# Optimization experiments

Measured on AMD Instinct MI355X. Metric: run time of the kernel, lower is better.

The kernel has to match this reference:

```python
import jax, jax.numpy as jnp
import numpy as np

B, N, E = 64, 1024, 16384   # graphs, nodes/graph, edges/graph
F, H, T, C = 128, 64, 10, 2 # input_dim, hid_dim, token_num, num_classes
INNER_PRUNE, CROSS_PRUNE = 0.3, 0.1
NEG_SLOPE = 0.01            # ProG act() defaults to leaky_relu


def setup_inputs() -> dict:
    key = jax.random.key(0)
    ks = jax.random.split(key, 8)
    x = jax.random.normal(ks[0], (B, N, F), jnp.float32)
    edge_src = jax.random.randint(ks[1], (B, E), 0, N, jnp.int32)
    edge_dst = jax.random.randint(ks[2], (B, E), 0, N, jnp.int32)
    # kaiming_uniform(leaky_relu, a=0.01, fan_in) for prompt tokens
    bound = float(np.sqrt(6.0 / ((1.0 + NEG_SLOPE ** 2) * F)))
    tokens = jax.random.uniform(ks[3], (T, F), jnp.float32, -bound, bound)

    def lin(k, fi, fo):
        b = 1.0 / np.sqrt(fi)
        k1, k2 = jax.random.split(k)
        return (jax.random.uniform(k1, (fi, fo), jnp.float32, -b, b),
                jax.random.uniform(k2, (fo,), jnp.float32, -b, b))

    W1, b1 = lin(ks[4], F, H)   # GCNConv 1
    W2, b2 = lin(ks[5], H, H)   # GCNConv 2
    Wa, ba = lin(ks[6], H, C)   # answering head
    return dict(x=x, tokens=tokens, W1=W1, b1=b1, W2=W2, b2=b2,
                Wa=Wa, ba=ba, edge_src=edge_src, edge_dst=edge_dst)


def reference(x, tokens, W1, b1, W2, b2, Wa, ba, edge_src, edge_dst):
    dt = x.dtype
    # --- HeavyPrompt: thresholded adjacency (edge existence only; PyG GCNConv
    # is called without edge_weight, so the sim values / edge_attr are unused)
    M_in = (jax.nn.sigmoid(tokens @ tokens.T) >= INNER_PRUNE).astype(dt)          # [T,T]
    M_cr = (jax.nn.sigmoid(jnp.einsum('tf,bnf->btn', tokens, x)) >= CROSS_PRUNE).astype(dt)  # [B,T,N], token->node

    # --- GCN normalization with self-loops (deg over targets)
    deg_tok = 1.0 + M_in.sum(0)                                                   # [T] (tokens only receive inner edges)
    offs = (jnp.arange(B, dtype=edge_dst.dtype) * N)[:, None]
    src_g = (edge_src + offs).reshape(-1)                                         # [B*E] global node ids
    dst_g = (edge_dst + offs).reshape(-1)
    in_deg = jax.ops.segment_sum(jnp.ones_like(dst_g, dt), dst_g, B * N).reshape(B, N)
    deg_node = 1.0 + in_deg + M_cr.sum(1)                                         # [B,N]
    inv_s_tok = jax.lax.rsqrt(deg_tok)
    inv_s_node = jax.lax.rsqrt(deg_node)
    inv_node_flat = inv_s_node.reshape(-1)
    norm_in = M_in * inv_s_tok[:, None] * inv_s_tok[None, :]                      # [T,T]
    ew = inv_node_flat[src_g] * inv_node_flat[dst_g]                              # per-edge 1/sqrt(di*dj)

    def gcn(ht, hn, W, b):
        # GCNConv: linear -> normalized aggregation (incl. self loop) -> +bias
        ht = ht @ W                                                               # [T,Fo] (token stream is graph-independent)
        hn = jnp.einsum('bnf,fo->bno', hn, W)                                     # [B,N,Fo]
        out_tok = norm_in @ ht + ht * (1.0 / deg_tok)[:, None] + b
        hn_flat = hn.reshape(B * N, -1)
        agg = jax.ops.segment_sum(hn_flat[src_g] * ew[:, None], dst_g, B * N).reshape(B, N, -1)
        cross = jnp.einsum('btn,to->bno', M_cr * inv_s_tok[None, :, None], ht) * inv_s_node[..., None]
        out_node = agg + cross + hn * (1.0 / deg_node)[..., None] + b
        return out_tok, out_node

    ht, hn = gcn(tokens, x, W1, b1)
    lrelu = lambda v: jnp.where(v >= 0, v, NEG_SLOPE * v)                         # act(); dropout is eval no-op
    ht, hn = lrelu(ht), lrelu(hn)
    ht, hn = gcn(ht, hn, W2, b2)                                                  # node_emb
    # global_mean_pool over each prompted graph (T tokens + N nodes)
    graph_emb = (ht.sum(0)[None, :] + hn.sum(1)) / (T + N)                        # [B,H]
    return jax.nn.softmax(graph_emb @ Wa + ba, axis=1)                            # answering
```

## Files before the change

kernel.cpp:

```cpp
#include <hip/hip_runtime.h>
#include <hip/hip_bf16.h>
#include <stdint.h>

#define B_ 64
#define N_ 1024
#define E_ 16384
#define F_ 128
#define H_ 64
#define T_ 10
#define BN (B_*N_)
#define BE (B_*E_)

#define TH_INNER (-0.84729786f)
#define TH_CROSS (-2.1972246f)

typedef __attribute__((ext_vector_type(8))) short short8;
typedef __attribute__((ext_vector_type(4))) float f32x4;

__device__ __forceinline__ float ld1(const void* p, int i, int bf) {
    if (bf) {
        uint16_t u = ((const uint16_t*)p)[i];
        return __uint_as_float(((uint32_t)u) << 16);
    }
    return ((const float*)p)[i];
}

__device__ __forceinline__ short to_bf(float x) {
    return (short)__bfloat16_as_ushort(__float2bfloat16(x));
}

__device__ __forceinline__ uint32_t pack_bf2(float lo, float hi) {
    uint32_t l = (uint32_t)__bfloat16_as_ushort(__float2bfloat16(lo));
    uint32_t h = (uint32_t)__bfloat16_as_ushort(__float2bfloat16(hi));
    return l | (h << 16);
}

__device__ __forceinline__ float bflo(uint32_t u) { return __uint_as_float(u << 16); }
__device__ __forceinline__ float bfhi(uint32_t u) { return __uint_as_float(u & 0xffff0000u); }

__global__ __launch_bounds__(1024) void k_count_prep(const int* __restrict__ dst,
                                                     int* __restrict__ cnt4,
                                                     const void* __restrict__ W1,
                                                     const void* __restrict__ W2,
                                                     const void* __restrict__ tokens,
                                                     int* __restrict__ flag,
                                                     short8* __restrict__ Bfr,
                                                     short8* __restrict__ Bfr2,
                                                     float* __restrict__ gsum,
                                                     uint32_t* __restrict__ y1pad,
                                                     uint32_t* __restrict__ y2pad) {
    __shared__ int lcnt[N_];
    int t = threadIdx.x;
    if (blockIdx.x >= 256) {
        uint32_t du = ((const uint32_t*)tokens)[t & 63];
        float dlo = __uint_as_float(du << 16);
        unsigned long long vote = __ballot(fabsf(dlo) <= 1.0f);
        int bf = (vote == ~0ull) ? 1 : 0;
        if (blockIdx.x == 256 && t == 0) *flag = bf;
        int f = (int)(blockIdx.x - 256) * 1024 + t;
        if (f < 1280) {
            int c = f / 320, rem = f % 320;
            int nt = rem / 64, lane = rem % 64;
            int q = lane >> 4, n = nt * 16 + (lane & 15);
            int k0 = c * 32 + q * 8;
            short8 v;
#pragma unroll
            for (int j = 0; j < 8; ++j) {
                int k = k0 + j;
                float x = 0.f;
                if (n < H_) x = ld1(W1, k * H_ + n, bf);
                else if (n < H_ + T_) x = ld1(tokens, (n - H_) * F_ + k, bf);
                v[j] = to_bf(x);
            }
            Bfr[f] = v;
        } else if (f < 1792) {
            int f2 = f - 1280;
            int c = f2 / 256, rem = f2 % 256;
            int nt = rem / 64, lane = rem % 64;
            int q = lane >> 4, n = nt * 16 + (lane & 15);
            int k0 = c * 32 + q * 8;
            short8 v;
#pragma unroll
            for (int j = 0; j < 8; ++j) v[j] = to_bf(ld1(W2, (k0 + j) * H_ + n, bf));
            Bfr2[f2] = v;
        }
        return;
    }
    int g = blockIdx.x & 63, c = blockIdx.x >> 6;
    lcnt[t] = 0;
    if (c == 0 && t < 64) gsum[g * 64 + t] = 0.f;
    if (blockIdx.x == 0) {
        if (t < 32) y1pad[t] = 0;
        else if (t < 64) y2pad[t - 32] = 0;
    }
    __syncthreads();
#pragma unroll
    for (int it = 0; it < 4; ++it)
        atomicAdd(&lcnt[dst[g * E_ + c * 4096 + it * 1024 + t]], 1);
    __syncthreads();
    cnt4[c * BN + g * N_ + t] = lcnt[t];
}

__global__ __launch_bounds__(1024) void k_scan_tok(const int* __restrict__ cnt4,
                                                   int* __restrict__ cnt,
                                                   int* __restrict__ offs,
                                                   int* __restrict__ base4,
                                                   const void* __restrict__ tokens,
                                                   const void* __restrict__ b1,
                                                   const void* __restrict__ b2,
                                                   const short8* __restrict__ Bfr,
                                                   const short8* __restrict__ Bfr2,
                                                   const int* __restrict__ flag,
                                                   uint32_t* __restrict__ y1,
                                                   uint32_t* __restrict__ y2,
                                                   float* __restrict__ tok_sum) {
    __shared__ int wsum[16];
    __shared__ float nm[T_ * 16];
    __shared__ float ist_s[16], idt_s[16];
    __shared__ float htbuf[T_ * 64];
    __shared__ float h1s[T_ * 64];
    int t = threadIdx.x;
    if (blockIdx.x < 64) {
        int g = blockIdx.x;
        int c0 = cnt4[0 * BN + g * N_ + t];
        int c1 = cnt4[1 * BN + g * N_ + t];
        int c2 = cnt4[2 * BN + g * N_ + t];
        int c3 = cnt4[3 * BN + g * N_ + t];
        int v = c0 + c1 + c2 + c3;
        int sc = v;
#pragma unroll
        for (int d = 1; d < 64; d <<= 1) {
            int u = __shfl_up(sc, d);
            if ((t & 63) >= d) sc += u;
        }
        if ((t & 63) == 63) wsum[t >> 6] = sc;
        __syncthreads();
        if (t < 16) {
            int wsc = wsum[t];
#pragma unroll
            for (int d = 1; d < 16; d <<= 1) {
                int u = __shfl_up(wsc, d);
                if (t >= d) wsc += u;
            }
            wsum[t] = wsc;
        }
        __syncthreads();
        int base = sc - v + ((t >= 64) ? wsum[(t >> 6) - 1] : 0);
        int o = g * E_ + base;
        cnt[g * N_ + t] = v;
        offs[g * N_ + t] = o;
        base4[0 * BN + g * N_ + t] = o;
        base4[1 * BN + g * N_ + t] = o + c0;
        base4[2 * BN + g * N_ + t] = o + c0 + c1;
        base4[3 * BN + g * N_ + t] = o + c0 + c1 + c2;
        return;
    }
    int bf = *flag;
    int l = t;
    bool act = (l < 64);
    int m = l & 15, q = (l & 63) >> 4;
    int mrow = (m < T_) ? m : (T_ - 1);
    f32x4 accM = {};
    f32x4 acc1[4] = {};
    float istc = 0.f, idtc = 0.f;
    if (act) {
        short8 afr[4];
        if (bf) {
            const short8* ar = (const short8*)((const uint16_t*)tokens + mrow * F_);
#pragma unroll
            for (int c = 0; c < 4; ++c) afr[c] = ar[c * 4 + q];
        } else {
            const float* ar = (const float*)tokens + mrow * F_;
#pragma unroll
            for (int c = 0; c < 4; ++c)
#pragma unroll
                for (int j = 0; j < 8; ++j) afr[c][j] = to_bf(ar[c * 32 + q * 8 + j]);
        }
#pragma unroll
        for (int c = 0; c < 4; ++c) {
            accM = __builtin_amdgcn_mfma_f32_16x16x32_bf16(afr[c], Bfr[(c * 5 + 4) * 64 + l], accM, 0, 0, 0);
#pragma unroll
            for (int nt = 0; nt < 4; ++nt)
                acc1[nt] = __builtin_amdgcn_mfma_f32_16x16x32_bf16(afr[c], Bfr[(c * 5 + nt) * 64 + l], acc1[nt], 0, 0, 0);
        }
        int ccnt = 0;
#pragma unroll
        for (int r = 0; r < 4; ++r) {
            int row = q * 4 + r;
            if (row < T_ && m < T_ && accM[r] >= TH_INNER) ccnt++;
        }
        ccnt += __shfl_xor(ccnt, 16);
        ccnt += __shfl_xor(ccnt, 32);
        float deg = 1.f + (float)ccnt;
        istc = 1.f / sqrtf(deg);
        idtc = 1.f / deg;
        if (q == 0 && m < T_) { ist_s[m] = istc; idt_s[m] = idtc; }
#pragma unroll
        for (int nt = 0; nt < 4; ++nt)
#pragma unroll
            for (int r = 0; r < 4; ++r) {
                int row = q * 4 + r;
                if (row < T_) htbuf[row * 64 + nt * 16 + m] = acc1[nt][r];
            }
    }
    __syncthreads();
    if (act && m < T_) {
#pragma unroll
        for (int r = 0; r < 4; ++r) {
            int row = q * 4 + r;
            if (row < T_)
                nm[row * 16 + m] = (accM[r] >= TH_INNER) ? ist_s[row] * istc : 0.f;
        }
    }
    __syncthreads();
    if (act) {
        float htc[T_];
#pragma unroll
        for (int s = 0; s < T_; ++s) htc[s] = htbuf[s * 64 + l];
        float b1f = ld1(b1, l, bf);
#pragma unroll
        for (int tt = 0; tt < T_; ++tt) {
            float a = htc[tt] * idt_s[tt] + b1f;
#pragma unroll
            for (int s = 0; s < T_; ++s) a += nm[tt * 16 + s] * htc[s];
            a = (a >= 0.f) ? a : 0.01f * a;
            h1s[tt * 64 + l] = a;
            float v = ist_s[tt] * htc[tt];
            float vh = __shfl(v, l + 1);
            if ((l & 1) == 0) y1[(size_t)(BN + 1 + tt) * 32 + (l >> 1)] = pack_bf2(v, vh);
        }
    }
    __syncthreads();
    if (act) {
        short8 a2fr[2];
#pragma unroll
        for (int c = 0; c < 2; ++c)
#pragma unroll
            for (int j = 0; j < 8; ++j) a2fr[c][j] = to_bf(h1s[mrow * 64 + c * 32 + q * 8 + j]);
        f32x4 acc2[4] = {};
#pragma unroll
        for (int nt = 0; nt < 4; ++nt)
#pragma unroll
            for (int c = 0; c < 2; ++c)
                acc2[nt] = __builtin_amdgcn_mfma_f32_16x16x32_bf16(a2fr[c], Bfr2[(c * 4 + nt) * 64 + l], acc2[nt], 0, 0, 0);
#pragma unroll
        for (int nt = 0; nt < 4; ++nt)
#pragma unroll
            for (int r = 0; r < 4; ++r) {
                int row = q * 4 + r;
                if (row < T_) htbuf[row * 64 + nt * 16 + m] = acc2[nt][r];
            }
    }
    __syncthreads();
    if (act) {
        float htc[T_];
#pragma unroll
        for (int s = 0; s < T_; ++s) htc[s] = htbuf[s * 64 + l];
        float b2f = ld1(b2, l, bf);
        float ts = 0.f;
#pragma unroll
        for (int tt = 0; tt < T_; ++tt) {
            float o = htc[tt] * idt_s[tt] + b2f;
#pragma unroll
            for (int s = 0; s < T_; ++s) o += nm[tt * 16 + s] * htc[s];
            ts += o;
            float v = ist_s[tt] * htc[tt];
            float vh = __shfl(v, l + 1);
            if ((l & 1) == 0) y2[(size_t)(BN + 1 + tt) * 32 + (l >> 1)] = pack_bf2(v, vh);
        }
        tok_sum[l] = ts;
    }
}

__global__ __launch_bounds__(1024) void k_scatter(const int* __restrict__ src,
                                                  const int* __restrict__ dst,
                                                  const int* __restrict__ base4,
                                                  int* __restrict__ bucket) {
    __shared__ int cur[N_];
    int t = threadIdx.x;
    int g = blockIdx.x & 63, c = blockIdx.x >> 6;
    cur[t] = base4[c * BN + g * N_ + t];
    __syncthreads();
#pragma unroll
    for (int it = 0; it < 4; ++it) {
        int i = g * E_ + c * 4096 + it * 1024 + t;
        int d = dst[i];
        int p = atomicAdd(&cur[d], 1);
        bucket[p] = g * N_ + src[i];
    }
}

__global__ __launch_bounds__(256) void k_node_mfma(const void* __restrict__ x,
                                                   const short8* __restrict__ Bfr,
                                                   const int* __restrict__ cnt,
                                                   const int* __restrict__ flag,
                                                   uint32_t* __restrict__ y1,
                                                   float* __restrict__ inv_s,
                                                   int* __restrict__ maskA) {
    int bf = *flag;
    int tid = threadIdx.x;
    int lane = tid & 63, wv = tid >> 6;
    int g = blockIdx.x & 63, c = blockIdx.x >> 6;
    int row0 = g * N_ + c * 64 + wv * 16;
    int m = lane & 15, q = lane >> 4;
    int row = row0 + m;
    short8 afr[4];
    if (bf) {
        const short8* ar = (const short8*)((const uint16_t*)x + (size_t)row * F_);
#pragma unroll
        for (int cc = 0; cc < 4; ++cc) afr[cc] = ar[cc * 4 + q];
    } else {
        const float* ar = (const float*)x + (size_t)row * F_;
#pragma unroll
        for (int cc = 0; cc < 4; ++cc)
#pragma unroll
            for (int j = 0; j < 8; ++j)
                afr[cc][j] = to_bf(ar[cc * 32 + q * 8 + j]);
    }
    f32x4 acc[5] = {};
#pragma unroll
    for (int nt = 0; nt < 5; ++nt)
#pragma unroll
        for (int cc = 0; cc < 4; ++cc) {
            short8 bfr = Bfr[(cc * 5 + nt) * 64 + lane];
            acc[nt] = __builtin_amdgcn_mfma_f32_16x16x32_bf16(afr[cc], bfr, acc[nt], 0, 0, 0);
        }
    unsigned long long bal[4];
#pragma unroll
    for (int r = 0; r < 4; ++r) {
        int pred = (m < T_) && (acc[4][r] >= TH_CROSS);
        bal[r] = __ballot(pred);
    }
    float isv[4];
#pragma unroll
    for (int r = 0; r < 4; ++r) {
        int node = row0 + q * 4 + r;
        int mk = (int)((bal[r] >> (q * 16)) & 0x3FF);
        int ec = cnt[node];
        int pc = __popc((unsigned)mk);
        float deg = 1.f + (float)ec + (float)pc;
        isv[r] = 1.f / sqrtf(deg);
        if (m == 0) { inv_s[node] = isv[r]; maskA[node] = mk; }
    }
#pragma unroll
    for (int r = 0; r < 4; ++r) {
        int node = row0 + q * 4 + r;
#pragma unroll
        for (int nt = 0; nt < 4; ++nt) {
            float v = acc[nt][r] * isv[r];
            float vh = __shfl(v, lane + 1);
            if ((m & 1) == 0)
                y1[(size_t)node * 32 + nt * 8 + (m >> 1)] = pack_bf2(v, vh);
        }
    }
}

#define NROWS (N_ + 12)

__device__ __forceinline__ void stage_slice(uint32_t* __restrict__ ys,
                                            const uint32_t* __restrict__ yg,
                                            const uint32_t* __restrict__ yall,
                                            int tid) {
#pragma unroll
    for (int it = 0; it < 9; ++it) {
        int idx = it * 1024 + tid;
        if (idx < NROWS * 8) {
            int r = idx >> 3, gg = idx & 7;
            const uint32_t* sp = (r < N_) ? (yg + r * 32)
                                          : (yall + (size_t)(BN + (r - N_)) * 32);
            *(uint4*)&ys[r * 32 + gg * 4] = *(const uint4*)(sp + gg * 4);
        }
    }
}

__device__ __forceinline__ void gather_grp(const uint32_t* __restrict__ ys,
                                           const int* __restrict__ bucket,
                                           int cnt_g, int off_g, int msk_g, int self_l,
                                           int wp, float a[8]) {
#pragma unroll
    for (int j = 0; j < 8; ++j) a[j] = 0.f;
    int cm = cnt_g;
    cm = max(cm, __shfl_xor(cm, 8));
    cm = max(cm, __shfl_xor(cm, 16));
    cm = max(cm, __shfl_xor(cm, 32));
    int nid0 = (cnt_g > 0) ? bucket[off_g] : 0;
    int nid1 = (cnt_g > 1) ? bucket[off_g + 1] : 0;
    for (int e = 0; e < cm; ++e) {
        int cur = nid0;
        nid0 = nid1;
        if (e + 2 < cnt_g) nid1 = bucket[off_g + e + 2];
        if (e < cnt_g) {
            int sl = cur & (N_ - 1);
            uint4 u = *(const uint4*)&ys[sl * 32 + wp * 4];
            a[0] += bflo(u.x); a[1] += bfhi(u.x);
            a[2] += bflo(u.y); a[3] += bfhi(u.y);
            a[4] += bflo(u.z); a[5] += bfhi(u.z);
            a[6] += bflo(u.w); a[7] += bfhi(u.w);
        }
    }
    unsigned mm = (unsigned)msk_g;
    while (mm) {
        int tk = __ffs(mm) - 1;
        mm &= mm - 1;
        uint4 u = *(const uint4*)&ys[(N_ + 1 + tk) * 32 + wp * 4];
        a[0] += bflo(u.x); a[1] += bfhi(u.x);
        a[2] += bflo(u.y); a[3] += bfhi(u.y);
        a[4] += bflo(u.z); a[5] += bfhi(u.z);
        a[6] += bflo(u.w); a[7] += bfhi(u.w);
    }
    {
        uint4 u = *(const uint4*)&ys[self_l * 32 + wp * 4];
        a[0] += bflo(u.x); a[1] += bfhi(u.x);
        a[2] += bflo(u.y); a[3] += bfhi(u.y);
        a[4] += bflo(u.z); a[5] += bfhi(u.z);
        a[6] += bflo(u.w); a[7] += bfhi(u.w);
    }
}

__global__ __launch_bounds__(1024, 1) void k_layer1(const uint32_t* __restrict__ y1,
                                                    const float* __restrict__ inv_s,
                                                    const int* __restrict__ cnt,
                                                    const int* __restrict__ offs,
                                                    const int* __restrict__ maskA,
                                                    const int* __restrict__ bucket,
                                                    const void* __restrict__ b1,
                                                    const short8* __restrict__ Bfr2,
                                                    const int* __restrict__ flag,
                                                    uint32_t* __restrict__ y2) {
    __shared__ uint32_t y1s[NROWS * 32];
    __shared__ uint32_t h1w[16][9 * 36];
    int bf = *flag;
    int tid = threadIdx.x;
    int lane = tid & 63, wv = tid >> 6;
    int gi = lane >> 3, wp = lane & 7;
    int g = blockIdx.x & 63, c = blockIdx.x >> 6;
    stage_slice(y1s, y1 + (size_t)g * N_ * 32, y1, tid);
    int nbase = g * N_ + c * 256 + wv * 16;
    int ln16 = lane & 15;
    int cntv = cnt[nbase + ln16];
    int offv = offs[nbase + ln16];
    float isvv = inv_s[nbase + ln16];
    int mskv = maskA[nbase + ln16];
    float bc[8];
#pragma unroll
    for (int j = 0; j < 8; ++j) bc[j] = ld1(b1, wp * 8 + j, bf);
    if (lane < 36) h1w[wv][8 * 36 + lane] = 0;
    __syncthreads();
    int m = lane & 15, q = lane >> 4;
    int mr = (m < 8) ? m : 8;
    for (int k = 0; k < 2; ++k) {
        int ni = k * 8 + gi;
        int cnt_g = __shfl(cntv, ni);
        int off_g = __shfl(offv, ni);
        int msk_g = __shfl(mskv, ni);
        float is_g = __shfl(isvv, ni);
        float a[8];
        gather_grp(y1s, bucket, cnt_g, off_g, msk_g, c * 256 + wv * 16 + ni, wp, a);
        uint32_t pk[4];
#pragma unroll
        for (int j = 0; j < 4; ++j) {
            float h0 = a[2 * j] * is_g + bc[2 * j];
            float h1v = a[2 * j + 1] * is_g + bc[2 * j + 1];
            h0 = (h0 >= 0.f) ? h0 : 0.01f * h0;
            h1v = (h1v >= 0.f) ? h1v : 0.01f * h1v;
            pk[j] = pack_bf2(h0, h1v);
        }
#pragma unroll
        for (int j = 0; j < 4; ++j) h1w[wv][gi * 36 + wp * 4 + j] = pk[j];
        short8 afr[2];
#pragma unroll
        for (int cc = 0; cc < 2; ++cc)
            afr[cc] = *(const short8*)&h1w[wv][mr * 36 + cc * 16 + q * 4];
        f32x4 acc[4] = {};
#pragma unroll
        for (int nt = 0; nt < 4; ++nt)
#pragma unroll
            for (int cc = 0; cc < 2; ++cc)
                acc[nt] = __builtin_amdgcn_mfma_f32_16x16x32_bf16(afr[cc], Bfr2[(cc * 4 + nt) * 64 + lane], acc[nt], 0, 0, 0);
#pragma unroll
        for (int r = 0; r < 4; ++r) {
            int tr = q * 4 + r;
            if (tr < 8) {
                int node = nbase + k * 8 + tr;
                float is = __shfl(isvv, k * 8 + tr);
#pragma unroll
                for (int nt = 0; nt < 4; ++nt) {
                    float v = acc[nt][r] * is;
                    float vh = __shfl(v, lane + 1);
                    if ((m & 1) == 0)
                        y2[(size_t)node * 32 + nt * 8 + (m >> 1)] = pack_bf2(v, vh);
                }
            }
        }
    }
}

__global__ __launch_bounds__(1024, 1) void k_layer2(const uint32_t* __restrict__ y2,
                                                    const float* __restrict__ inv_s,
                                                    const int* __restrict__ cnt,
                                                    const int* __restrict__ offs,
                                                    const int* __restrict__ maskA,
                                                    const int* __restrict__ bucket,
                                                    const void* __restrict__ b2,
                                                    const int* __restrict__ flag,
                                                    float* __restrict__ graph_sum) {
    __shared__ uint32_t y2s[NROWS * 32];
    __shared__ float pool[16][64];
    int bf = *flag;
    int tid = threadIdx.x;
    int lane = tid & 63, wv = tid >> 6;
    int gi = lane >> 3, wp = lane & 7;
    int g = blockIdx.x & 63, c = blockIdx.x >> 6;
    stage_slice(y2s, y2 + (size_t)g * N_ * 32, y2, tid);
    int nbase = g * N_ + c * 256 + wv * 16;
    int ln16 = lane & 15;
    int cntv = cnt[nbase + ln16];
    int offv = offs[nbase + ln16];
    float isvv = inv_s[nbase + ln16];
    int mskv = maskA[nbase + ln16];
    float bc[8];
#pragma unroll
    for (int j = 0; j < 8; ++j) bc[j] = ld1(b2, wp * 8 + j, bf);
    __syncthreads();
    float p[8];
#pragma unroll
    for (int j = 0; j < 8; ++j) p[j] = 0.f;
    for (int k = 0; k < 2; ++k) {
        int ni = k * 8 + gi;
        int cnt_g = __shfl(cntv, ni);
        int off_g = __shfl(offv, ni);
        int msk_g = __shfl(mskv, ni);
        float is_g = __shfl(isvv, ni);
        float a[8];
        gather_grp(y2s, bucket, cnt_g, off_g, msk_g, c * 256 + wv * 16 + ni, wp, a);
#pragma unroll
        for (int j = 0; j < 8; ++j) p[j] += a[j] * is_g + bc[j];
    }
#pragma unroll
    for (int j = 0; j < 8; ++j) {
        p[j] += __shfl_xor(p[j], 8);
        p[j] += __shfl_xor(p[j], 16);
        p[j] += __shfl_xor(p[j], 32);
    }
    if (gi == 0) {
#pragma unroll
        for (int j = 0; j < 8; ++j) pool[wv][wp * 8 + j] = p[j];
    }
    __syncthreads();
    if (tid < 64) {
        float s = 0.f;
#pragma unroll
        for (int w2 = 0; w2 < 16; ++w2) s += pool[w2][tid];
        atomicAdd(&graph_sum[g * H_ + tid], s);
    }
}

__global__ __launch_bounds__(64) void k_final(const float* __restrict__ graph_sum,
                                              const float* __restrict__ tok_sum,
                                              const void* __restrict__ Wa,
                                              const void* __restrict__ ba,
                                              const int* __restrict__ flag,
                                              void* __restrict__ out) {
    int bf = *flag;
    int b = blockIdx.x, l = threadIdx.x;
    float e = (tok_sum[l] + graph_sum[b * H_ + l]) * (1.0f / 1034.0f);
    float p0 = e * ld1(Wa, l * 2 + 0, bf);
    float p1 = e * ld1(Wa, l * 2 + 1, bf);
#pragma unroll
    for (int d = 32; d >= 1; d >>= 1) {
        p0 += __shfl_xor(p0, d);
        p1 += __shfl_xor(p1, d);
    }
    if (l == 0) {
        float l0 = p0 + ld1(ba, 0, bf);
        float l1 = p1 + ld1(ba, 1, bf);
        float mx = fmaxf(l0, l1);
        float e0 = expf(l0 - mx), e1 = expf(l1 - mx);
        float s = e0 + e1;
        float o0 = e0 / s, o1 = e1 / s;
        if (bf) {
            ((__hip_bfloat16*)out)[b * 2 + 0] = __float2bfloat16(o0);
            ((__hip_bfloat16*)out)[b * 2 + 1] = __float2bfloat16(o1);
        } else {
            ((float*)out)[b * 2 + 0] = o0;
            ((float*)out)[b * 2 + 1] = o1;
        }
    }
}

extern "C" void kernel_launch(void* const* d_in, const int* in_sizes, int n_in,
                              void* d_out, int out_size, void* d_ws, size_t ws_size,
                              hipStream_t stream) {
    (void)in_sizes; (void)n_in; (void)out_size; (void)ws_size;
    const void* x      = d_in[0];
    const void* tokens = d_in[1];
    const void* W1     = d_in[2];
    const void* b1     = d_in[3];
    const void* W2     = d_in[4];
    const void* b2     = d_in[5];
    const void* Wa     = d_in[6];
    const void* ba     = d_in[7];
    const int* esrc = (const int*)d_in[8];
    const int* edst = (const int*)d_in[9];

    char* w = (char*)d_ws;
    auto alloc = [&](size_t bytes) { void* p = (void*)w; w += (bytes + 255) & ~(size_t)255; return p; };
    int*      cnt       = (int*)alloc(BN * 4);
    int*      offs      = (int*)alloc(BN * 4);
    int*      maskA     = (int*)alloc(BN * 4);
    float*    inv_s     = (float*)alloc(BN * 4);
    int*      cnt4      = (int*)alloc((size_t)4 * BN * 4);
    int*      base4     = (int*)alloc((size_t)4 * BN * 4);
    int*      bucket    = (int*)alloc((size_t)BE * 4 + 512);
    uint32_t* y1        = (uint32_t*)alloc((size_t)(BN + 12) * 32 * 4);
    uint32_t* y2        = (uint32_t*)alloc((size_t)(BN + 12) * 32 * 4);
    float*    tok_sum   = (float*)alloc(H_ * 4);
    float*    graph_sum = (float*)alloc(B_ * H_ * 4);
    short8*   Bfr       = (short8*)alloc(4 * 5 * 64 * sizeof(short8));
    short8*   Bfr2      = (short8*)alloc(2 * 4 * 64 * sizeof(short8));
    int*      dflag     = (int*)alloc(256);

    k_count_prep<<<258, 1024, 0, stream>>>(edst, cnt4, W1, W2, tokens, dflag, Bfr, Bfr2,
                                           graph_sum, y1 + (size_t)BN * 32, y2 + (size_t)BN * 32);
    k_scan_tok  <<<65, 1024, 0, stream>>>(cnt4, cnt, offs, base4, tokens, b1, b2,
                                          Bfr, Bfr2, dflag, y1, y2, tok_sum);
    k_scatter   <<<256, 1024, 0, stream>>>(esrc, edst, base4, bucket);
    k_node_mfma <<<BN / 64, 256, 0, stream>>>(x, Bfr, cnt, dflag, y1, inv_s, maskA);
    k_layer1    <<<B_ * 4, 1024, 0, stream>>>(y1, inv_s, cnt, offs, maskA, bucket, b1, Bfr2, dflag, y2);
    k_layer2    <<<B_ * 4, 1024, 0, stream>>>(y2, inv_s, cnt, offs, maskA, bucket, b2, dflag, graph_sum);
    k_final     <<<B_, 64, 0, stream>>>(graph_sum, tok_sum, Wa, ba, dflag, d_out);
}
```

Baseline: 160.0 us.

## Fuse scatter with node MFMA and fold final softmax into layer2 via tickets

Merges the edge-scatter kernel and the node MFMA projection into one launch with block-index dispatch, moving the MFMA part to 1024-thread blocks covering 256 rows each. The final softmax head now runs inside layer2: the last of four blocks per graph, found with a ticket counter, computes the output. The neighbour-gather loop also drops its wave-wide max-count loop bound and per-iteration guard. Together these remove two kernel launches and some divergent iterations, at the cost of an atomic ticket, a threadfence and larger node blocks with possibly lower occupancy.

```diff
diff --git a/kernel.cpp b/kernel.cpp
--- a/kernel.cpp
+++ b/kernel.cpp
@@ -47,6 +47,7 @@
                                                      short8* __restrict__ Bfr,
                                                      short8* __restrict__ Bfr2,
                                                      float* __restrict__ gsum,
+                                                     int* __restrict__ done,
                                                      uint32_t* __restrict__ y1pad,
                                                      uint32_t* __restrict__ y2pad) {
     __shared__ int lcnt[N_];
@@ -92,6 +93,7 @@
     if (blockIdx.x == 0) {
         if (t < 32) y1pad[t] = 0;
         else if (t < 64) y2pad[t - 32] = 0;
+        else if (t >= 128 && t < 192) done[t - 128] = 0;
     }
     __syncthreads();
 #pragma unroll
@@ -162,7 +164,7 @@
     int mrow = (m < T_) ? m : (T_ - 1);
     f32x4 accM = {};
     f32x4 acc1[4] = {};
-    float istc = 0.f, idtc = 0.f;
+    float istc = 0.f;
     if (act) {
         short8 afr[4];
         if (bf) {
@@ -193,8 +195,7 @@
         ccnt += __shfl_xor(ccnt, 32);
         float deg = 1.f + (float)ccnt;
         istc = 1.f / sqrtf(deg);
-        idtc = 1.f / deg;
-        if (q == 0 && m < T_) { ist_s[m] = istc; idt_s[m] = idtc; }
+        if (q == 0 && m < T_) { ist_s[m] = istc; idt_s[m] = 1.f / deg; }
 #pragma unroll
         for (int nt = 0; nt < 4; ++nt)
 #pragma unroll
@@ -272,36 +273,37 @@
     }
 }
 
-__global__ __launch_bounds__(1024) void k_scatter(const int* __restrict__ src,
-                                                  const int* __restrict__ dst,
-                                                  const int* __restrict__ base4,
-                                                  int* __restrict__ bucket) {
+__global__ __launch_bounds__(1024) void k_scatter_node(const int* __restrict__ src,
+                                                       const int* __restrict__ dst,
+                                                       const int* __restrict__ base4,
+                                                       int* __restrict__ bucket,
+                                                       const void* __restrict__ x,
+                                                       const short8* __restrict__ Bfr,
+                                                       const int* __restrict__ cnt,
+                                                       const int* __restrict__ flag,
+                                                       uint32_t* __restrict__ y1,
+                                                       float* __restrict__ inv_s,
+                                                       int* __restrict__ maskA) {
     __shared__ int cur[N_];
     int t = threadIdx.x;
-    int g = blockIdx.x & 63, c = blockIdx.x >> 6;
-    cur[t] = base4[c * BN + g * N_ + t];
-    __syncthreads();
-#pragma unroll
-    for (int it = 0; it < 4; ++it) {
-        int i = g * E_ + c * 4096 + it * 1024 + t;
-        int d = dst[i];
-        int p = atomicAdd(&cur[d], 1);
-        bucket[p] = g * N_ + src[i];
-    }
-}
-
-__global__ __launch_bounds__(256) void k_node_mfma(const void* __restrict__ x,
-                                                   const short8* __restrict__ Bfr,
-                                                   const int* __restrict__ cnt,
-                                                   const int* __restrict__ flag,
-                                                   uint32_t* __restrict__ y1,
-                                                   float* __restrict__ inv_s,
-                                                   int* __restrict__ maskA) {
+    if (blockIdx.x < 256) {
+        int g = blockIdx.x & 63, c = blockIdx.x >> 6;
+        cur[t] = base4[c * BN + g * N_ + t];
+        __syncthreads();
+#pragma unroll
+        for (int it = 0; it < 4; ++it) {
+            int i = g * E_ + c * 4096 + it * 1024 + t;
+            int d = dst[i];
+            int p = atomicAdd(&cur[d], 1);
+            bucket[p] = g * N_ + src[i];
+        }
+        return;
+    }
+    int bid = blockIdx.x - 256;
     int bf = *flag;
-    int tid = threadIdx.x;
-    int lane = tid & 63, wv = tid >> 6;
-    int g = blockIdx.x & 63, c = blockIdx.x >> 6;
-    int row0 = g * N_ + c * 64 + wv * 16;
+    int lane = t & 63, w16 = t >> 6;
+    int g = bid & 63, c = bid >> 6;
+    int row0 = g * N_ + c * 256 + w16 * 16;
     int m = lane & 15, q = lane >> 4;
     int row = row0 + m;
     short8 afr[4];
@@ -379,24 +381,18 @@
                                            int wp, float a[8]) {
 #pragma unroll
     for (int j = 0; j < 8; ++j) a[j] = 0.f;
-    int cm = cnt_g;
-    cm = max(cm, __shfl_xor(cm, 8));
-    cm = max(cm, __shfl_xor(cm, 16));
-    cm = max(cm, __shfl_xor(cm, 32));
     int nid0 = (cnt_g > 0) ? bucket[off_g] : 0;
     int nid1 = (cnt_g > 1) ? bucket[off_g + 1] : 0;
-    for (int e = 0; e < cm; ++e) {
-        int cur = nid0;
+    for (int e = 0; e < cnt_g; ++e) {
+        int curN = nid0;
         nid0 = nid1;
         if (e + 2 < cnt_g) nid1 = bucket[off_g + e + 2];
-        if (e < cnt_g) {
-            int sl = cur & (N_ - 1);
-            uint4 u = *(const uint4*)&ys[sl * 32 + wp * 4];
-            a[0] += bflo(u.x); a[1] += bfhi(u.x);
-            a[2] += bflo(u.y); a[3] += bfhi(u.y);
-            a[4] += bflo(u.z); a[5] += bfhi(u.z);
-            a[6] += bflo(u.w); a[7] += bfhi(u.w);
-        }
+        int sl = curN & (N_ - 1);
+        uint4 u = *(const uint4*)&ys[sl * 32 + wp * 4];
+        a[0] += bflo(u.x); a[1] += bfhi(u.x);
+        a[2] += bflo(u.y); a[3] += bfhi(u.y);
+        a[4] += bflo(u.z); a[5] += bfhi(u.z);
+        a[6] += bflo(u.w); a[7] += bfhi(u.w);
     }
     unsigned mm = (unsigned)msk_g;
     while (mm) {
@@ -503,9 +499,15 @@
                                                     const int* __restrict__ bucket,
                                                     const void* __restrict__ b2,
                                                     const int* __restrict__ flag,
-                                                    float* __restrict__ graph_sum) {
+                                                    float* __restrict__ graph_sum,
+                                                    int* __restrict__ done,
+                                                    const float* __restrict__ tok_sum,
+                                                    const void* __restrict__ Wa,
+                                                    const void* __restrict__ ba,
+                                                    void* __restrict__ out) {
     __shared__ uint32_t y2s[NROWS * 32];
     __shared__ float pool[16][64];
+    __shared__ int ticket_s;
     int bf = *flag;
     int tid = threadIdx.x;
     int lane = tid & 63, wv = tid >> 6;
@@ -553,37 +555,34 @@
         for (int w2 = 0; w2 < 16; ++w2) s += pool[w2][tid];
         atomicAdd(&graph_sum[g * H_ + tid], s);
     }
-}
-
-__global__ __launch_bounds__(64) void k_final(const float* __restrict__ graph_sum,
-                                              const float* __restrict__ tok_sum,
-                                              const void* __restrict__ Wa,
-                                              const void* __restrict__ ba,
-                                              const int* __restrict__ flag,
-                                              void* __restrict__ out) {
-    int bf = *flag;
-    int b = blockIdx.x, l = threadIdx.x;
-    float e = (tok_sum[l] + graph_sum[b * H_ + l]) * (1.0f / 1034.0f);
-    float p0 = e * ld1(Wa, l * 2 + 0, bf);
-    float p1 = e * ld1(Wa, l * 2 + 1, bf);
-#pragma unroll
-    for (int d = 32; d >= 1; d >>= 1) {
-        p0 += __shfl_xor(p0, d);
-        p1 += __shfl_xor(p1, d);
-    }
-    if (l == 0) {
-        float l0 = p0 + ld1(ba, 0, bf);
-        float l1 = p1 + ld1(ba, 1, bf);
-        float mx = fmaxf(l0, l1);
-        float e0 = expf(l0 - mx), e1 = expf(l1 - mx);
-        float s = e0 + e1;
-        float o0 = e0 / s, o1 = e1 / s;
-        if (bf) {
-            ((__hip_bfloat16*)out)[b * 2 + 0] = __float2bfloat16(o0);
-            ((__hip_bfloat16*)out)[b * 2 + 1] = __float2bfloat16(o1);
-        } else {
-            ((float*)out)[b * 2 + 0] = o0;
-            ((float*)out)[b * 2 + 1] = o1;
+    __threadfence();
+    if (tid == 0) ticket_s = atomicAdd(&done[g], 1);
+    __syncthreads();
+    if (ticket_s == 3 && tid < 64) {
+        int l = tid;
+        float gs = atomicAdd(&graph_sum[g * H_ + l], 0.0f);
+        float e = (tok_sum[l] + gs) * (1.0f / 1034.0f);
+        float p0 = e * ld1(Wa, l * 2 + 0, bf);
+        float p1 = e * ld1(Wa, l * 2 + 1, bf);
+#pragma unroll
+        for (int d = 32; d >= 1; d >>= 1) {
+            p0 += __shfl_xor(p0, d);
+            p1 += __shfl_xor(p1, d);
+        }
+        if (l == 0) {
+            float l0 = p0 + ld1(ba, 0, bf);
+            float l1 = p1 + ld1(ba, 1, bf);
+            float mx = fmaxf(l0, l1);
+            float e0 = expf(l0 - mx), e1 = expf(l1 - mx);
+            float s = e0 + e1;
+            float o0 = e0 / s, o1 = e1 / s;
+            if (bf) {
+                ((__hip_bfloat16*)out)[g * 2 + 0] = __float2bfloat16(o0);
+                ((__hip_bfloat16*)out)[g * 2 + 1] = __float2bfloat16(o1);
+            } else {
+                ((float*)out)[g * 2 + 0] = o0;
+                ((float*)out)[g * 2 + 1] = o1;
+            }
         }
     }
 }
@@ -616,17 +615,19 @@
     uint32_t* y2        = (uint32_t*)alloc((size_t)(BN + 12) * 32 * 4);
     float*    tok_sum   = (float*)alloc(H_ * 4);
     float*    graph_sum = (float*)alloc(B_ * H_ * 4);
+    int*      done      = (int*)alloc(B_ * 4);
     short8*   Bfr       = (short8*)alloc(4 * 5 * 64 * sizeof(short8));
     short8*   Bfr2      = (short8*)alloc(2 * 4 * 64 * sizeof(short8));
     int*      dflag     = (int*)alloc(256);
 
-    k_count_prep<<<258, 1024, 0, stream>>>(edst, cnt4, W1, W2, tokens, dflag, Bfr, Bfr2,
-                                           graph_sum, y1 + (size_t)BN * 32, y2 + (size_t)BN * 32);
-    k_scan_tok  <<<65, 1024, 0, stream>>>(cnt4, cnt, offs, base4, tokens, b1, b2,
-                                          Bfr, Bfr2, dflag, y1, y2, tok_sum);
-    k_scatter   <<<256, 1024, 0, stream>>>(esrc, edst, base4, bucket);
-    k_node_mfma <<<BN / 64, 256, 0, stream>>>(x, Bfr, cnt, dflag, y1, inv_s, maskA);
-    k_layer1    <<<B_ * 4, 1024, 0, stream>>>(y1, inv_s, cnt, offs, maskA, bucket, b1, Bfr2, dflag, y2);
-    k_layer2    <<<B_ * 4, 1024, 0, stream>>>(y2, inv_s, cnt, offs, maskA, bucket, b2, dflag, graph_sum);
-    k_final     <<<B_, 64, 0, stream>>>(graph_sum, tok_sum, Wa, ba, dflag, d_out);
-}
+    k_count_prep  <<<258, 1024, 0, stream>>>(edst, cnt4, W1, W2, tokens, dflag, Bfr, Bfr2,
+                                             graph_sum, done,
+                                             y1 + (size_t)BN * 32, y2 + (size_t)BN * 32);
+    k_scan_tok    <<<65, 1024, 0, stream>>>(cnt4, cnt, offs, base4, tokens, b1, b2,
+                                            Bfr, Bfr2, dflag, y1, y2, tok_sum);
+    k_scatter_node<<<512, 1024, 0, stream>>>(esrc, edst, base4, bucket, x, Bfr, cnt,
+                                             dflag, y1, inv_s, maskA);
+    k_layer1      <<<B_ * 4, 1024, 0, stream>>>(y1, inv_s, cnt, offs, maskA, bucket, b1, Bfr2, dflag, y2);
+    k_layer2      <<<B_ * 4, 1024, 0, stream>>>(y2, inv_s, cnt, offs, maskA, bucket, b2, dflag,
+                                                graph_sum, done, tok_sum, Wa, ba, d_out);
+}
```

Measured after the change: 209.7 us. 1.31x slower.
